# Optimization experiments

Measured on AMD Instinct MI355X. Metric: run time of the kernel, lower is better.

The kernel has to match this reference:

```python
import jax, jax.numpy as jnp
import numpy as np

B = 4096
P = 10000          # points per cloud (hard-coded view(-1,3,10000))
NUM_POINTS = 100   # forced by phi.view(-1, 300)
BOX_SIZE = 0.5
H_G = 128
H_L = 128


def setup_inputs() -> dict:
    key = jax.random.key(0)
    ks = jax.random.split(key, 12)
    x = jax.random.uniform(ks[0], (B, 3, P, 1), dtype=jnp.float32)
    l_t_prev = jax.random.uniform(ks[1], (B, 3), dtype=jnp.float32)
    sc = 0.02
    W1 = jax.random.normal(ks[2], (H_G, NUM_POINTS * 3), dtype=jnp.float32) * sc
    b1 = jnp.zeros((H_G,), jnp.float32)
    W2 = jax.random.normal(ks[3], (H_L, 3), dtype=jnp.float32) * sc
    b2 = jnp.zeros((H_L,), jnp.float32)
    W3 = jax.random.normal(ks[4], (H_G + H_L, H_G), dtype=jnp.float32) * sc
    b3 = jnp.zeros((H_G + H_L,), jnp.float32)
    W4 = jax.random.normal(ks[5], (H_G + H_L, H_L), dtype=jnp.float32) * sc
    b4 = jnp.zeros((H_G + H_L,), jnp.float32)
    return {"x": x, "l_t_prev": l_t_prev, "W1": W1, "b1": b1, "W2": W2,
            "b2": b2, "W3": W3, "b3": b3, "W4": W4, "b4": b4}


def _foveate(x, l):
    # x: (B,3,P,1) -> pts: (B,3,P)
    pts = x.reshape(x.shape[0], 3, P)
    half = BOX_SIZE / 2.0
    lo = l - half  # (B,3)
    hi = l + half
    # per-point in-box mask over all 3 axes: (B,P)
    inside = jnp.all((pts >= lo[:, :, None]) & (pts <= hi[:, :, None]), axis=1)
    count = inside.sum(axis=-1)  # (B,)
    # stable argsort puts in-box point indices first, preserving order
    order = jnp.argsort(~inside, axis=-1, stable=True)  # (B,P)
    pos = jnp.arange(NUM_POINTS)
    # deterministic stand-in for random subsample/pad: take first NUM_POINTS
    # in-box points, wrapping (repeating) if fewer than NUM_POINTS exist
    safe = pos[None, :] % jnp.maximum(count, 1)[:, None]  # (B,NUM_POINTS)
    idx = jnp.take_along_axis(order, safe, axis=-1)  # (B,NUM_POINTS)
    idx3 = jnp.broadcast_to(idx[:, None, :], (pts.shape[0], 3, NUM_POINTS))
    sel = jnp.take_along_axis(pts, idx3, axis=2)  # (B,3,NUM_POINTS)
    # empty boxes -> zero fill (matches torch.zeros fill_box branch)
    sel = jnp.where(count[:, None, None] > 0, sel, jnp.zeros_like(sel))
    return sel.reshape(pts.shape[0], 3 * NUM_POINTS)  # (B,300)


def reference(x, l_t_prev, W1, b1, W2, b2, W3, b3, W4, b4):
    phi = _foveate(x, l_t_prev)                       # (B,300)
    phi_out = jax.nn.relu(phi @ W1.T + b1)            # (B,h_g)
    l_out = jax.nn.relu(l_t_prev @ W2.T + b2)         # (B,h_l)
    what = phi_out @ W3.T + b3                        # (B,h_g+h_l)
    where = l_out @ W4.T + b4                         # (B,h_g+h_l)
    return jax.nn.relu(what + where)
```

## Files before the change

### kernel.cpp

```cpp
#include <hip/hip_runtime.h>

#define NPTS 100
#define P_F4 2500

__global__ __launch_bounds__(256) void foveate_kernel(
    const float* __restrict__ x,
    const float* __restrict__ l,
    float* __restrict__ phiT,
    int B)
{
    const int tid  = threadIdx.x;
    const int wv   = tid >> 6;
    const int lane = tid & 63;
    const int b    = blockIdx.x * 4 + wv;

    __shared__ float s_phi[4][300];

    const float lx = l[b * 3 + 0];
    const float ly = l[b * 3 + 1];
    const float lz = l[b * 3 + 2];
    const float lox = lx - 0.25f, hix = lx + 0.25f;
    const float loy = ly - 0.25f, hiy = ly + 0.25f;
    const float loz = lz - 0.25f, hiz = lz + 0.25f;

    const float4* xr = (const float4*)(x + (size_t)b * 30000);

    int fc = (lane < P_F4) ? lane : (P_F4 - 1);
    float4 a = xr[fc], c = xr[P_F4 + fc], d = xr[2 * P_F4 + fc];

    int cnt = 0;
    for (int base = 0; base < P_F4; base += 64) {
        const int  f0 = base + lane;
        const bool v  = (f0 < P_F4);
        const float4 ca = a, cc = c, cd = d;
        if (base + 64 < P_F4) {
            int nf = base + 64 + lane;
            int nfc = (nf < P_F4) ? nf : (P_F4 - 1);
            a = xr[nfc]; c = xr[P_F4 + nfc]; d = xr[2 * P_F4 + nfc];
        }
        const bool in0 = v && ca.x >= lox && ca.x <= hix && cc.x >= loy && cc.x <= hiy && cd.x >= loz && cd.x <= hiz;
        const bool in1 = v && ca.y >= lox && ca.y <= hix && cc.y >= loy && cc.y <= hiy && cd.y >= loz && cd.y <= hiz;
        const bool in2 = v && ca.z >= lox && ca.z <= hix && cc.z >= loy && cc.z <= hiy && cd.z >= loz && cd.z <= hiz;
        const bool in3 = v && ca.w >= lox && ca.w <= hix && cc.w >= loy && cc.w <= hiy && cd.w >= loz && cd.w <= hiz;

        const unsigned long long m0 = __ballot(in0);
        const unsigned long long m1 = __ballot(in1);
        const unsigned long long m2 = __ballot(in2);
        const unsigned long long m3 = __ballot(in3);
        const unsigned long long below = (1ull << lane) - 1ull;

        int pos = cnt + __popcll(m0 & below) + __popcll(m1 & below) +
                        __popcll(m2 & below) + __popcll(m3 & below);
        if (in0) { if (pos < NPTS) { s_phi[wv][pos] = ca.x; s_phi[wv][NPTS + pos] = cc.x; s_phi[wv][2 * NPTS + pos] = cd.x; } ++pos; }
        if (in1) { if (pos < NPTS) { s_phi[wv][pos] = ca.y; s_phi[wv][NPTS + pos] = cc.y; s_phi[wv][2 * NPTS + pos] = cd.y; } ++pos; }
        if (in2) { if (pos < NPTS) { s_phi[wv][pos] = ca.z; s_phi[wv][NPTS + pos] = cc.z; s_phi[wv][2 * NPTS + pos] = cd.z; } ++pos; }
        if (in3) { if (pos < NPTS) { s_phi[wv][pos] = ca.w; s_phi[wv][NPTS + pos] = cc.w; s_phi[wv][2 * NPTS + pos] = cd.w; } ++pos; }

        cnt += __popcll(m0) + __popcll(m1) + __popcll(m2) + __popcll(m3);
        if (cnt >= NPTS) break;
    }

    __syncthreads();

    const int n = (cnt < NPTS) ? cnt : NPTS;
    if (n == 0) {
        for (int j = lane; j < 3 * NPTS; j += 64) s_phi[wv][j] = 0.0f;
    } else if (n < NPTS) {
        for (int j = n + lane; j < NPTS; j += 64) {
            const int src = j % n;
            s_phi[wv][j]            = s_phi[wv][src];
            s_phi[wv][NPTS + j]     = s_phi[wv][NPTS + src];
            s_phi[wv][2 * NPTS + j] = s_phi[wv][2 * NPTS + src];
        }
    }
    __syncthreads();

    for (int i = lane; i < 3 * NPTS; i += 64)
        phiT[(size_t)i * B + b] = s_phi[wv][i];
}

__global__ __launch_bounds__(256) void mlp1_kernel(
    const float* __restrict__ phiT,
    const float* __restrict__ l,
    const float* __restrict__ W1,
    const float* __restrict__ b1,
    const float* __restrict__ W2,
    const float* __restrict__ b2,
    float* __restrict__ h1T,
    float* __restrict__ loT,
    int B)
{
    const int tid  = threadIdx.x;
    const int wv   = tid >> 6;
    const int lane = tid & 63;
    const int BG   = B >> 6;
    const int bg   = blockIdx.x % BG;
    const int kh   = blockIdx.x / BG;
    const int col  = bg * 64 + lane;
    const int k0   = __builtin_amdgcn_readfirstlane(kh * 64 + wv * 16);

    float acc[16];
    #pragma unroll
    for (int kk = 0; kk < 16; ++kk) acc[kk] = b1[k0 + kk];

    const float* __restrict__ w1 = W1 + (size_t)k0 * 300;
    #pragma unroll 4
    for (int i = 0; i < 300; ++i) {
        const float pv = phiT[(size_t)i * B + col];
        #pragma unroll
        for (int kk = 0; kk < 16; ++kk)
            acc[kk] = fmaf(pv, w1[kk * 300 + i], acc[kk]);
    }
    #pragma unroll
    for (int kk = 0; kk < 16; ++kk)
        h1T[(size_t)(k0 + kk) * B + col] = fmaxf(acc[kk], 0.0f);

    const float l0 = l[col * 3 + 0];
    const float l1 = l[col * 3 + 1];
    const float l2 = l[col * 3 + 2];
    #pragma unroll
    for (int kk = 0; kk < 16; ++kk) {
        const int k = k0 + kk;
        const float lo = b2[k] + l0 * W2[k * 3 + 0] + l1 * W2[k * 3 + 1] + l2 * W2[k * 3 + 2];
        loT[(size_t)k * B + col] = fmaxf(lo, 0.0f);
    }
}

__global__ __launch_bounds__(256) void mlp2_kernel(
    const float* __restrict__ h1T,
    const float* __restrict__ loT,
    const float* __restrict__ W3,
    const float* __restrict__ b3,
    const float* __restrict__ W4,
    const float* __restrict__ b4,
    float* __restrict__ out,
    int B)
{
    const int tid  = threadIdx.x;
    const int wv   = tid >> 6;
    const int lane = tid & 63;
    const int BG   = B >> 6;
    const int bg   = blockIdx.x % BG;
    const int mq   = blockIdx.x / BG;
    const int col  = bg * 64 + lane;
    const int m0   = __builtin_amdgcn_readfirstlane(mq * 64 + wv * 16);

    float acc[16];
    #pragma unroll
    for (int kk = 0; kk < 16; ++kk) acc[kk] = b3[m0 + kk] + b4[m0 + kk];

    const float* __restrict__ w3 = W3 + (size_t)m0 * 128;
    const float* __restrict__ w4 = W4 + (size_t)m0 * 128;
    #pragma unroll 2
    for (int k = 0; k < 128; ++k) {
        const float hv = h1T[(size_t)k * B + col];
        const float lv = loT[(size_t)k * B + col];
        #pragma unroll
        for (int kk = 0; kk < 16; ++kk)
            acc[kk] = fmaf(hv, w3[kk * 128 + k], fmaf(lv, w4[kk * 128 + k], acc[kk]));
    }

    __shared__ float s_o[64][65];
    #pragma unroll
    for (int kk = 0; kk < 16; ++kk)
        s_o[wv * 16 + kk][lane] = fmaxf(acc[kk], 0.0f);
    __syncthreads();
    #pragma unroll
    for (int r = 0; r < 16; ++r) {
        const int bb = wv * 16 + r;
        out[(size_t)(bg * 64 + bb) * 256 + mq * 64 + lane] = s_o[lane][bb];
    }
}

extern "C" void kernel_launch(void* const* d_in, const int* in_sizes, int n_in,
                              void* d_out, int out_size, void* d_ws, size_t ws_size,
                              hipStream_t stream) {
    const float* x  = (const float*)d_in[0];
    const float* l  = (const float*)d_in[1];
    const float* W1 = (const float*)d_in[2];
    const float* b1 = (const float*)d_in[3];
    const float* W2 = (const float*)d_in[4];
    const float* b2 = (const float*)d_in[5];
    const float* W3 = (const float*)d_in[6];
    const float* b3 = (const float*)d_in[7];
    const float* W4 = (const float*)d_in[8];
    const float* b4 = (const float*)d_in[9];
    float* out = (float*)d_out;

    const int B = in_sizes[1] / 3;

    float* phiT = (float*)d_ws;
    float* h1T  = phiT + (size_t)300 * B;
    float* loT  = h1T  + (size_t)128 * B;

    foveate_kernel<<<B / 4, 256, 0, stream>>>(x, l, phiT, B);
    mlp1_kernel<<<2 * (B / 64), 256, 0, stream>>>(phiT, l, W1, b1, W2, b2, h1T, loT, B);
    mlp2_kernel<<<4 * (B / 64), 256, 0, stream>>>(h1T, loT, W3, b3, W4, b4, out, B);
}
```

Measured before the change: 685.5 us.

## Use float4-interleaved intermediates, one-wave foveate blocks, and finer MLP work split

The intermediate activations are now stored as float4 groups of four features per batch column, so the MLP kernels do vectorized loads and stores. The foveate kernel runs one wave per block and prefetches two iterations ahead. Both MLP kernels now compute fewer output features per wave (4 and 8) across more blocks, which raises occupancy at the cost of more redundant activation reads. mlp2 drops its shared-memory transpose and writes float4 rows straight to the output.

New measurement: 637.7 us. 1.07x faster.

```diff
diff --git a/kernel.cpp b/kernel.cpp
--- a/kernel.cpp
+++ b/kernel.cpp
@@ -3,18 +3,16 @@
 #define NPTS 100
 #define P_F4 2500
 
-__global__ __launch_bounds__(256) void foveate_kernel(
+__global__ __launch_bounds__(64) void foveate_kernel(
     const float* __restrict__ x,
     const float* __restrict__ l,
-    float* __restrict__ phiT,
+    float4* __restrict__ phi4,
     int B)
 {
-    const int tid  = threadIdx.x;
-    const int wv   = tid >> 6;
-    const int lane = tid & 63;
-    const int b    = blockIdx.x * 4 + wv;
-
-    __shared__ float s_phi[4][300];
+    const int lane = threadIdx.x;
+    const int b    = blockIdx.x;
+
+    __shared__ __align__(16) float s_phi[3 * NPTS];
 
     const float lx = l[b * 3 + 0];
     const float ly = l[b * 3 + 1];
@@ -25,18 +23,19 @@
 
     const float4* xr = (const float4*)(x + (size_t)b * 30000);
 
-    int fc = (lane < P_F4) ? lane : (P_F4 - 1);
-    float4 a = xr[fc], c = xr[P_F4 + fc], d = xr[2 * P_F4 + fc];
+    float4 a0 = xr[lane], c0 = xr[P_F4 + lane], d0 = xr[2 * P_F4 + lane];
+    int nf1 = 64 + lane; int nc1 = (nf1 < P_F4) ? nf1 : (P_F4 - 1);
+    float4 a1 = xr[nc1], c1 = xr[P_F4 + nc1], d1 = xr[2 * P_F4 + nc1];
 
     int cnt = 0;
     for (int base = 0; base < P_F4; base += 64) {
-        const int  f0 = base + lane;
-        const bool v  = (f0 < P_F4);
-        const float4 ca = a, cc = c, cd = d;
-        if (base + 64 < P_F4) {
-            int nf = base + 64 + lane;
+        const bool v = (base + lane < P_F4);
+        const float4 ca = a0, cc = c0, cd = d0;
+        a0 = a1; c0 = c1; d0 = d1;
+        if (base + 128 < P_F4) {
+            int nf = base + 128 + lane;
             int nfc = (nf < P_F4) ? nf : (P_F4 - 1);
-            a = xr[nfc]; c = xr[P_F4 + nfc]; d = xr[2 * P_F4 + nfc];
+            a1 = xr[nfc]; c1 = xr[P_F4 + nfc]; d1 = xr[2 * P_F4 + nfc];
         }
         const bool in0 = v && ca.x >= lox && ca.x <= hix && cc.x >= loy && cc.x <= hiy && cd.x >= loz && cd.x <= hiz;
         const bool in1 = v && ca.y >= lox && ca.y <= hix && cc.y >= loy && cc.y <= hiy && cd.y >= loz && cd.y <= hiz;
@@ -51,10 +50,10 @@
 
         int pos = cnt + __popcll(m0 & below) + __popcll(m1 & below) +
                         __popcll(m2 & below) + __popcll(m3 & below);
-        if (in0) { if (pos < NPTS) { s_phi[wv][pos] = ca.x; s_phi[wv][NPTS + pos] = cc.x; s_phi[wv][2 * NPTS + pos] = cd.x; } ++pos; }
-        if (in1) { if (pos < NPTS) { s_phi[wv][pos] = ca.y; s_phi[wv][NPTS + pos] = cc.y; s_phi[wv][2 * NPTS + pos] = cd.y; } ++pos; }
-        if (in2) { if (pos < NPTS) { s_phi[wv][pos] = ca.z; s_phi[wv][NPTS + pos] = cc.z; s_phi[wv][2 * NPTS + pos] = cd.z; } ++pos; }
-        if (in3) { if (pos < NPTS) { s_phi[wv][pos] = ca.w; s_phi[wv][NPTS + pos] = cc.w; s_phi[wv][2 * NPTS + pos] = cd.w; } ++pos; }
+        if (in0) { if (pos < NPTS) { s_phi[pos] = ca.x; s_phi[NPTS + pos] = cc.x; s_phi[2 * NPTS + pos] = cd.x; } ++pos; }
+        if (in1) { if (pos < NPTS) { s_phi[pos] = ca.y; s_phi[NPTS + pos] = cc.y; s_phi[2 * NPTS + pos] = cd.y; } ++pos; }
+        if (in2) { if (pos < NPTS) { s_phi[pos] = ca.z; s_phi[NPTS + pos] = cc.z; s_phi[2 * NPTS + pos] = cd.z; } ++pos; }
+        if (in3) { if (pos < NPTS) { s_phi[pos] = ca.w; s_phi[NPTS + pos] = cc.w; s_phi[2 * NPTS + pos] = cd.w; } ++pos; }
 
         cnt += __popcll(m0) + __popcll(m1) + __popcll(m2) + __popcll(m3);
         if (cnt >= NPTS) break;
@@ -64,30 +63,31 @@
 
     const int n = (cnt < NPTS) ? cnt : NPTS;
     if (n == 0) {
-        for (int j = lane; j < 3 * NPTS; j += 64) s_phi[wv][j] = 0.0f;
+        for (int j = lane; j < 3 * NPTS; j += 64) s_phi[j] = 0.0f;
     } else if (n < NPTS) {
         for (int j = n + lane; j < NPTS; j += 64) {
             const int src = j % n;
-            s_phi[wv][j]            = s_phi[wv][src];
-            s_phi[wv][NPTS + j]     = s_phi[wv][NPTS + src];
-            s_phi[wv][2 * NPTS + j] = s_phi[wv][2 * NPTS + src];
+            s_phi[j]            = s_phi[src];
+            s_phi[NPTS + j]     = s_phi[NPTS + src];
+            s_phi[2 * NPTS + j] = s_phi[2 * NPTS + src];
         }
     }
     __syncthreads();
 
-    for (int i = lane; i < 3 * NPTS; i += 64)
-        phiT[(size_t)i * B + b] = s_phi[wv][i];
+    const float4* sp = (const float4*)s_phi;
+    for (int g = lane; g < 75; g += 64)
+        phi4[(size_t)g * B + b] = sp[g];
 }
 
 __global__ __launch_bounds__(256) void mlp1_kernel(
-    const float* __restrict__ phiT,
+    const float4* __restrict__ phi4,
     const float* __restrict__ l,
     const float* __restrict__ W1,
     const float* __restrict__ b1,
     const float* __restrict__ W2,
     const float* __restrict__ b2,
-    float* __restrict__ h1T,
-    float* __restrict__ loT,
+    float4* __restrict__ h14,
+    float4* __restrict__ lo4,
     int B)
 {
     const int tid  = threadIdx.x;
@@ -97,38 +97,45 @@
     const int bg   = blockIdx.x % BG;
     const int kh   = blockIdx.x / BG;
     const int col  = bg * 64 + lane;
-    const int k0   = __builtin_amdgcn_readfirstlane(kh * 64 + wv * 16);
-
-    float acc[16];
+    const int k0   = __builtin_amdgcn_readfirstlane(kh * 16 + wv * 4);
+
+    float acc[4];
     #pragma unroll
-    for (int kk = 0; kk < 16; ++kk) acc[kk] = b1[k0 + kk];
+    for (int kk = 0; kk < 4; ++kk) acc[kk] = b1[k0 + kk];
 
     const float* __restrict__ w1 = W1 + (size_t)k0 * 300;
-    #pragma unroll 4
-    for (int i = 0; i < 300; ++i) {
-        const float pv = phiT[(size_t)i * B + col];
+    #pragma unroll 5
+    for (int g = 0; g < 75; ++g) {
+        const float4 p = phi4[(size_t)g * B + col];
         #pragma unroll
-        for (int kk = 0; kk < 16; ++kk)
-            acc[kk] = fmaf(pv, w1[kk * 300 + i], acc[kk]);
-    }
-    #pragma unroll
-    for (int kk = 0; kk < 16; ++kk)
-        h1T[(size_t)(k0 + kk) * B + col] = fmaxf(acc[kk], 0.0f);
+        for (int kk = 0; kk < 4; ++kk) {
+            const float* __restrict__ wr = w1 + kk * 300 + 4 * g;
+            acc[kk] = fmaf(p.x, wr[0], acc[kk]);
+            acc[kk] = fmaf(p.y, wr[1], acc[kk]);
+            acc[kk] = fmaf(p.z, wr[2], acc[kk]);
+            acc[kk] = fmaf(p.w, wr[3], acc[kk]);
+        }
+    }
+    float4 h;
+    h.x = fmaxf(acc[0], 0.0f); h.y = fmaxf(acc[1], 0.0f);
+    h.z = fmaxf(acc[2], 0.0f); h.w = fmaxf(acc[3], 0.0f);
+    h14[(size_t)(k0 >> 2) * B + col] = h;
 
     const float l0 = l[col * 3 + 0];
     const float l1 = l[col * 3 + 1];
     const float l2 = l[col * 3 + 2];
+    float lo[4];
     #pragma unroll
-    for (int kk = 0; kk < 16; ++kk) {
+    for (int kk = 0; kk < 4; ++kk) {
         const int k = k0 + kk;
-        const float lo = b2[k] + l0 * W2[k * 3 + 0] + l1 * W2[k * 3 + 1] + l2 * W2[k * 3 + 2];
-        loT[(size_t)k * B + col] = fmaxf(lo, 0.0f);
-    }
+        lo[kk] = fmaxf(b2[k] + l0 * W2[k * 3 + 0] + l1 * W2[k * 3 + 1] + l2 * W2[k * 3 + 2], 0.0f);
+    }
+    lo4[(size_t)(k0 >> 2) * B + col] = make_float4(lo[0], lo[1], lo[2], lo[3]);
 }
 
 __global__ __launch_bounds__(256) void mlp2_kernel(
-    const float* __restrict__ h1T,
-    const float* __restrict__ loT,
+    const float4* __restrict__ h14,
+    const float4* __restrict__ lo4,
     const float* __restrict__ W3,
     const float* __restrict__ b3,
     const float* __restrict__ W4,
@@ -143,33 +150,34 @@
     const int bg   = blockIdx.x % BG;
     const int mq   = blockIdx.x / BG;
     const int col  = bg * 64 + lane;
-    const int m0   = __builtin_amdgcn_readfirstlane(mq * 64 + wv * 16);
-
-    float acc[16];
+    const int m0   = __builtin_amdgcn_readfirstlane(mq * 32 + wv * 8);
+
+    float acc[8];
     #pragma unroll
-    for (int kk = 0; kk < 16; ++kk) acc[kk] = b3[m0 + kk] + b4[m0 + kk];
+    for (int mm = 0; mm < 8; ++mm) acc[mm] = b3[m0 + mm] + b4[m0 + mm];
 
     const float* __restrict__ w3 = W3 + (size_t)m0 * 128;
     const float* __restrict__ w4 = W4 + (size_t)m0 * 128;
-    #pragma unroll 2
-    for (int k = 0; k < 128; ++k) {
-        const float hv = h1T[(size_t)k * B + col];
-        const float lv = loT[(size_t)k * B + col];
+    #pragma unroll 4
+    for (int kb = 0; kb < 32; ++kb) {
+        const float4 h = h14[(size_t)kb * B + col];
+        const float4 v = lo4[(size_t)kb * B + col];
         #pragma unroll
-        for (int kk = 0; kk < 16; ++kk)
-            acc[kk] = fmaf(hv, w3[kk * 128 + k], fmaf(lv, w4[kk * 128 + k], acc[kk]));
-    }
-
-    __shared__ float s_o[64][65];
-    #pragma unroll
-    for (int kk = 0; kk < 16; ++kk)
-        s_o[wv * 16 + kk][lane] = fmaxf(acc[kk], 0.0f);
-    __syncthreads();
-    #pragma unroll
-    for (int r = 0; r < 16; ++r) {
-        const int bb = wv * 16 + r;
-        out[(size_t)(bg * 64 + bb) * 256 + mq * 64 + lane] = s_o[lane][bb];
-    }
+        for (int mm = 0; mm < 8; ++mm) {
+            const float* __restrict__ r3 = w3 + mm * 128 + 4 * kb;
+            const float* __restrict__ r4 = w4 + mm * 128 + 4 * kb;
+            acc[mm] = fmaf(h.x, r3[0], fmaf(v.x, r4[0], acc[mm]));
+            acc[mm] = fmaf(h.y, r3[1], fmaf(v.y, r4[1], acc[mm]));
+            acc[mm] = fmaf(h.z, r3[2], fmaf(v.z, r4[2], acc[mm]));
+            acc[mm] = fmaf(h.w, r3[3], fmaf(v.w, r4[3], acc[mm]));
+        }
+    }
+
+    float4* orow = (float4*)(out + (size_t)col * 256 + m0);
+    orow[0] = make_float4(fmaxf(acc[0], 0.0f), fmaxf(acc[1], 0.0f),
+                          fmaxf(acc[2], 0.0f), fmaxf(acc[3], 0.0f));
+    orow[1] = make_float4(fmaxf(acc[4], 0.0f), fmaxf(acc[5], 0.0f),
+                          fmaxf(acc[6], 0.0f), fmaxf(acc[7], 0.0f));
 }
 
 extern "C" void kernel_launch(void* const* d_in, const int* in_sizes, int n_in,
@@ -193,7 +201,9 @@
     float* h1T  = phiT + (size_t)300 * B;
     float* loT  = h1T  + (size_t)128 * B;
 
-    foveate_kernel<<<B / 4, 256, 0, stream>>>(x, l, phiT, B);
-    mlp1_kernel<<<2 * (B / 64), 256, 0, stream>>>(phiT, l, W1, b1, W2, b2, h1T, loT, B);
-    mlp2_kernel<<<4 * (B / 64), 256, 0, stream>>>(h1T, loT, W3, b3, W4, b4, out, B);
-}
+    foveate_kernel<<<B, 64, 0, stream>>>(x, l, (float4*)phiT, B);
+    mlp1_kernel<<<8 * (B / 64), 256, 0, stream>>>((const float4*)phiT, l, W1, b1, W2, b2,
+                                                  (float4*)h1T, (float4*)loT, B);
+    mlp2_kernel<<<8 * (B / 64), 256, 0, stream>>>((const float4*)h1T, (const float4*)loT,
+                                                  W3, b3, W4, b4, out, B);
+}
```
